# Kernel tuning notes

Hardware: AMD Instinct MI355X
Metric: run time of the kernel (lower is better)

## Reference

```python
import jax, jax.numpy as jnp
import numpy as np

B, T = 2048, 2048
VOCAB, E, H = 32000, 4, 4


def _gru_layer(x, Wih, Whh, bih, bhh, reverse=False):
    """PyTorch-semantics GRU over batch_first x [B,T,F]; returns [B,T,H]."""
    Bn = x.shape[0]
    Hn = Whh.shape[1]
    # Precompute input projections for all timesteps: [B,T,3H]
    xi = jnp.einsum('btf,gf->btg', x, Wih) + bih
    if reverse:
        xi = xi[:, ::-1]
    xi_t = jnp.swapaxes(xi, 0, 1)  # [T,B,3H]

    def step(h, xt):
        gh = h @ Whh.T + bhh                      # [B,3H]
        xr, xz, xn = jnp.split(xt, 3, axis=-1)
        hr, hz, hn = jnp.split(gh, 3, axis=-1)
        r = jax.nn.sigmoid(xr + hr)
        z = jax.nn.sigmoid(xz + hz)
        n = jnp.tanh(xn + r * hn)
        h_new = (1.0 - z) * n + z * h
        return h_new, h_new

    h0 = jnp.zeros((Bn, Hn), x.dtype)
    _, ys = jax.lax.scan(step, h0, xi_t)
    ys = jnp.swapaxes(ys, 0, 1)  # [B,T,H]
    if reverse:
        ys = ys[:, ::-1]
    return ys


def setup_inputs() -> dict:
    key = jax.random.key(0)
    ks = jax.random.split(key, 16)
    x = jax.random.randint(ks[0], (B, T), 0, VOCAB, dtype=jnp.int64)
    s = 0.3  # xavier-ish scale for tiny dims
    emb   = jax.random.normal(ks[1], (VOCAB, E), jnp.float32) * s
    Wih_f = jax.random.normal(ks[2], (3 * H, E), jnp.float32) * s
    Whh_f = jax.random.normal(ks[3], (3 * H, H), jnp.float32) * s
    Wih_b = jax.random.normal(ks[4], (3 * H, E), jnp.float32) * s
    Whh_b = jax.random.normal(ks[5], (3 * H, H), jnp.float32) * s
    Wih_o = jax.random.normal(ks[6], (3 * 1, 2 * H), jnp.float32) * s
    Whh_o = jax.random.normal(ks[7], (3 * 1, 1), jnp.float32) * s
    z = jnp.zeros
    return {
        'x': x, 'emb': emb,
        'Wih_f': Wih_f, 'Whh_f': Whh_f, 'bih_f': z((3 * H,)), 'bhh_f': z((3 * H,)),
        'Wih_b': Wih_b, 'Whh_b': Whh_b, 'bih_b': z((3 * H,)), 'bhh_b': z((3 * H,)),
        'Wih_o': Wih_o, 'Whh_o': Whh_o, 'bih_o': z((3,)), 'bhh_o': z((3,)),
    }


def reference(x, emb, Wih_f, Whh_f, bih_f, bhh_f, Wih_b, Whh_b, bih_b, bhh_b,
              Wih_o, Whh_o, bih_o, bhh_o):
    h = emb[x]                                         # [B,T,E]
    fwd = _gru_layer(h, Wih_f, Whh_f, bih_f, bhh_f, reverse=False)
    bwd = _gru_layer(h, Wih_b, Whh_b, bih_b, bhh_b, reverse=True)
    bi = jnp.concatenate([fwd, bwd], axis=-1)          # [B,T,2H]
    out = _gru_layer(bi, Wih_o, Whh_o, bih_o, bhh_o)   # [B,T,1]
    return jax.nn.sigmoid(out).reshape(x.shape[0], -1) # [B,T]
```

## Files before the change

kernel.cpp:

```cpp
#include <hip/hip_runtime.h>
#include <hip/hip_bf16.h>
#include <hip/hip_fp16.h>


#define NB 2048
#define NT 2048
#define NV 32000
#define PA_CH 32
#define PA_CL 64
#define PA_WUP 24
#define PB_CH 64
#define PB_CL 32
#define PB_WUP 16
#define CH 32
#define CL (NT / CH)
#define WUP 64

#define W_EMB    0
#define W_WIH_F  128000
#define W_WHH_F  128048
#define W_BIH_F  128096
#define W_BHH_F  128108
#define W_WIH_B  128120
#define W_WHH_B  128168
#define W_BIH_B  128216
#define W_BHH_B  128228
#define W_WIH_O  128240
#define W_WHH_O  128264
#define W_BIH_O  128267
#define W_BHH_O  128270
#define W_TOTAL  128273

static constexpr size_t WBLK_BYTES = 524288;
static constexpr size_t XIH_BYTES  = (size_t)NV * 16 * 2;
static constexpr size_t D_BYTES    = (size_t)NT * NB * 8;
static constexpr size_t XT_BYTES   = (size_t)NT * NB * 2;
static constexpr size_t N2_XIH_F   = WBLK_BYTES;
static constexpr size_t N2_XIH_B   = N2_XIH_F + XIH_BYTES;
static constexpr size_t N2_DF      = N2_XIH_B + XIH_BYTES;
static constexpr size_t N2_DB      = N2_DF + D_BYTES;
static constexpr size_t N2_XT      = N2_DB + D_BYTES;
static constexpr size_t NEED_NEW2  = N2_XT + XT_BYTES;
static constexpr size_t XI_STRIDE  = 16;
static constexpr size_t XI_BYTES   = (size_t)NV * XI_STRIDE * 4;
static constexpr size_t HS_BYTES   = (size_t)NT * NB * 4 * 2;
static constexpr size_t OFF_XI_F   = WBLK_BYTES;
static constexpr size_t OFF_XI_B   = OFF_XI_F + XI_BYTES;
static constexpr size_t OFF_HS_B   = OFF_XI_B + XI_BYTES;
static constexpr size_t OFF_HS_F   = OFF_HS_B + HS_BYTES;
static constexpr size_t NEED_XI    = OFF_HS_B;
static constexpr size_t NEED_FAST  = OFF_HS_F + HS_BYTES;

__device__ __forceinline__ float frcp_(float x) { return __builtin_amdgcn_rcpf(x); }
__device__ __forceinline__ float sigm_(float x) { return frcp_(1.f + __expf(-x)); }
__device__ __forceinline__ float tanh_(float x) { return 1.f - 2.f * frcp_(1.f + __expf(2.f * x)); }
__device__ __forceinline__ float b2f_(__hip_bfloat16 v) { return __bfloat162float(v); }
__device__ __forceinline__ unsigned f2bf_(float f) {
  __hip_bfloat16 h = __float2bfloat16(f);
  return (unsigned)__builtin_bit_cast(unsigned short, h);
}
__device__ __forceinline__ unsigned pack2_(float a, float b) { return f2bf_(a) | (f2bf_(b) << 16); }
__device__ __forceinline__ float bflo_(unsigned u) { return __builtin_bit_cast(float, u << 16); }
__device__ __forceinline__ float bfhi_(unsigned u) { return __builtin_bit_cast(float, u & 0xffff0000u); }
__device__ __forceinline__ float2 h2f2_(unsigned u) {
  __half2 h = __builtin_bit_cast(__half2, u);
  return __half22float2(h);
}
__device__ __forceinline__ unsigned packh2_(float a, float b) {
  __half2 h = __floats2half2_rn(a, b);
  return __builtin_bit_cast(unsigned, h);
}

__device__ __forceinline__ int probe_is_bf16_(const void* emb) {
  const unsigned short* u = (const unsigned short*)emb;
  int sane = 0;
#pragma unroll
  for (int i = 0; i < 64; ++i) {
    unsigned short v = u[2 * i];
    unsigned e = (v >> 7) & 0xff;
    sane += (e >= 107 && e <= 146) || ((v & 0x7fff) == 0);
  }
  return sane >= 48;
}
__device__ __forceinline__ int probe_x_is64_(const int* x) {
  int zeros = 0;
#pragma unroll
  for (int i = 0; i < 32; ++i) zeros += (x[2 * i + 1] == 0);
  return zeros >= 28;
}
__device__ __forceinline__ int tok_(const int* x, size_t idx, int is64) {
  return is64 ? x[idx * 2] : x[idx];
}
__device__ __forceinline__ float ldf_(const void* p, int i, int isb) {
  return isb ? b2f_(((const __hip_bfloat16*)p)[i]) : ((const float*)p)[i];
}

__global__ void prep_fused_kernel(const int* __restrict__ x,
                                  const void* emb, const void* Wih_f, const void* Whh_f,
                                  const void* bih_f, const void* bhh_f,
                                  const void* Wih_b, const void* Whh_b,
                                  const void* bih_b, const void* bhh_b,
                                  const void* Wih_o, const void* Whh_o,
                                  const void* bih_o, const void* bhh_o,
                                  __half* __restrict__ xih_f, __half* __restrict__ xih_b,
                                  unsigned short* __restrict__ xT, float* __restrict__ W) {
  __shared__ int tile[64][65];
  const int blk = blockIdx.x;
  if (blk < 251) {
    const int tid = blk * 256 + (int)threadIdx.x;
    if (tid >= 2 * NV) return;
    const int isb = probe_is_bf16_(emb);
    const int dir = (tid >= NV) ? 1 : 0;
    const int v = dir ? tid - NV : tid;
    const void* Wih = dir ? Wih_b : Wih_f;
    const void* bih = dir ? bih_b : bih_f;
    const void* bhh = dir ? bhh_b : bhh_f;
    char* dst = (char*)((dir ? xih_b : xih_f) + (size_t)v * 16);
    const float e0 = ldf_(emb, v * 4 + 0, isb), e1 = ldf_(emb, v * 4 + 1, isb);
    const float e2 = ldf_(emb, v * 4 + 2, isb), e3 = ldf_(emb, v * 4 + 3, isb);
    float g[12];
#pragma unroll
    for (int gi = 0; gi < 12; ++gi) {
      float s = ldf_(bih, gi, isb) + (gi < 8 ? ldf_(bhh, gi, isb) : 0.f);
      s += ldf_(Wih, gi * 4 + 0, isb) * e0 + ldf_(Wih, gi * 4 + 1, isb) * e1 +
           ldf_(Wih, gi * 4 + 2, isb) * e2 + ldf_(Wih, gi * 4 + 3, isb) * e3;
      g[gi] = s;
    }
    uint4 qa, qb;
    qa.x = packh2_(g[0], g[1]);  qa.y = packh2_(g[2], g[3]);
    qa.z = packh2_(g[4], g[5]);  qa.w = packh2_(g[6], g[7]);
    qb.x = packh2_(g[8], g[9]);  qb.y = packh2_(g[10], g[11]);
    qb.z = 0u; qb.w = 0u;
    *(uint4*)(dst) = qa;
    *(uint4*)(dst + 16) = qb;
  } else if (blk < 1275) {
    const int x64 = probe_x_is64_(x);
    const int bi2 = blk - 251;
    const int tb = bi2 & 31;
    const int tt = bi2 >> 5;
    const int b0 = tb * 64, t0 = tt * 64;
    const int r = (int)threadIdx.x >> 2;
    const int s = (int)threadIdx.x & 3;
    const int bb = b0 + r;
    if (x64) {
      const uint4* p = (const uint4*)(x + ((size_t)bb * NT + t0 + s * 16) * 2);
#pragma unroll
      for (int i = 0; i < 8; ++i) {
        uint4 q = p[i];
        tile[r][s * 16 + 2 * i] = (int)q.x;
        tile[r][s * 16 + 2 * i + 1] = (int)q.z;
      }
    } else {
      const uint4* p = (const uint4*)(x + (size_t)bb * NT + t0 + s * 16);
#pragma unroll
      for (int i = 0; i < 4; ++i) {
        uint4 q = p[i];
        const int base = s * 16 + 4 * i;
        tile[r][base] = (int)q.x; tile[r][base + 1] = (int)q.y;
        tile[r][base + 2] = (int)q.z; tile[r][base + 3] = (int)q.w;
      }
    }
    __syncthreads();
    const int tx = (int)threadIdx.x & 63, ty = (int)threadIdx.x >> 6;
#pragma unroll
    for (int j = 0; j < 16; ++j) {
      const int t = t0 + ty + 4 * j;
      xT[(size_t)t * NB + b0 + tx] = (unsigned short)tile[tx][ty + 4 * j];
    }
  } else {
    const int i0 = (int)threadIdx.x;
    if (i0 >= W_TOTAL - W_WHH_F) return;
    const int isb = probe_is_bf16_(emb);
    const int i = W_WHH_F + i0;
    const void* src; int off;
    if      (i < W_BIH_F) { src = Whh_f; off = i - W_WHH_F; }
    else if (i < W_BHH_F) { src = bih_f; off = i - W_BIH_F; }
    else if (i < W_WIH_B) { src = bhh_f; off = i - W_BHH_F; }
    else if (i < W_WHH_B) { src = Wih_b; off = i - W_WIH_B; }
    else if (i < W_BIH_B) { src = Whh_b; off = i - W_WHH_B; }
    else if (i < W_BHH_B) { src = bih_b; off = i - W_BIH_B; }
    else if (i < W_WIH_O) { src = bhh_b; off = i - W_BHH_B; }
    else if (i < W_WHH_O) { src = Wih_o; off = i - W_WIH_O; }
    else if (i < W_BIH_O) { src = Whh_o; off = i - W_WHH_O; }
    else if (i < W_BHH_O) { src = bih_o; off = i - W_BIH_O; }
    else                  { src = bhh_o; off = i - W_BHH_O; }
    W[i] = ldf_(src, off, isb);
  }
}

__global__ void __launch_bounds__(64, 2)
gru_scan_p5(const unsigned short* __restrict__ xT, const float* __restrict__ W,
            const __half* __restrict__ xih_f, const __half* __restrict__ xih_b,
            unsigned* __restrict__ df, unsigned* __restrict__ db) {
  const int bi = blockIdx.x;
  const int rg = bi & 31;
  const int c = (bi >> 5) & (PA_CH - 1);
  const int dir = bi >> 10;
  const int b = rg * 64 + (int)threadIdx.x;
  const char* __restrict__ xib = (const char*)(dir ? xih_b : xih_f);
  const char* __restrict__ xtb = (const char*)xT;
  char* __restrict__ dsb = (char*)(dir ? db : df);
  const float* Whh = W + (dir ? W_WHH_B : W_WHH_F);
  const float* bhh = W + (dir ? W_BHH_B : W_BHH_F);

  float w[12][4];
#pragma unroll
  for (int g = 0; g < 12; ++g)
#pragma unroll
    for (int k = 0; k < 4; ++k) w[g][k] = Whh[g * 4 + k];
  float bn[4];
#pragma unroll
  for (int j = 0; j < 4; ++j) bn[j] = bhh[8 + j];
  float wr4[4], wz4[4], wn4[4];
#pragma unroll
  for (int k = 0; k < 4; ++k) {
    wr4[k] = W[W_WIH_O + dir * 4 + k];
    wz4[k] = W[W_WIH_O + 8 + dir * 4 + k];
    wn4[k] = W[W_WIH_O + 16 + dir * 4 + k];
  }

  const int lo = c * PA_CL, hi = lo + PA_CL;
  int t0, d, wsteps;
  if (dir == 0) {
    d = 1;
    t0 = (c == 0) ? 0 : lo - PA_WUP;
    wsteps = (c == 0) ? 0 : PA_WUP;
  } else {
    d = -1;
    t0 = (c == PA_CH - 1) ? NT - 1 : hi - 1 + PA_WUP;
    wsteps = (c == PA_CH - 1) ? 0 : PA_WUP;
  }

#define CLMP(tt_) ((tt_) < 0 ? 0 : ((tt_) > NT - 1 ? NT - 1 : (tt_)))

  uint4 XA[8], XB[8];
  int KT[8];
#pragma unroll
  for (int j = 0; j < 8; ++j) {
    const int tj = CLMP(t0 + j * d);
    const unsigned kj = (unsigned)xT[(size_t)tj * NB + b] << 5;
    XA[j] = *(const uint4*)(xib + kj);
    XB[j] = *(const uint4*)(xib + kj + 16);
  }
#pragma unroll
  for (int j = 0; j < 8; ++j) {
    const int tj = CLMP(t0 + (8 + j) * d);
    KT[j] = (int)xT[(size_t)tj * NB + b];
  }

  const int dtok = d * (NB * 2);
  const int otlo = b * 2, othi = (NT - 1) * (NB * 2) + b * 2;
  int otok = CLMP(t0 + 16 * d) * (NB * 2) + b * 2;

  float h[4] = {0.f, 0.f, 0.f, 0.f};
  int odot = 0;
  const int ddot = d * (NB * 8);

#define ASTEP(J, DO_STORE)                                                     \
  {                                                                            \
    const unsigned ko = (unsigned)KT[J] << 5;                                  \
    const uint4 A = XA[J];                                                     \
    const uint4 Bq = XB[J];                                                    \
    XA[J] = *(const uint4*)(xib + ko);                                         \
    XB[J] = *(const uint4*)(xib + ko + 16);                                    \
    KT[J] = (int)*(const unsigned short*)(xtb + otok);                         \
    otok += dtok;                                                              \
    otok = otok < otlo ? otlo : (otok > othi ? othi : otok);                   \
    const float2 r01 = h2f2_(A.x), r23 = h2f2_(A.y);                           \
    const float2 z01 = h2f2_(A.z), z23 = h2f2_(A.w);                           \
    const float2 n01 = h2f2_(Bq.x), n23 = h2f2_(Bq.y);                         \
    const float xr[4] = {r01.x, r01.y, r23.x, r23.y};                          \
    const float xz[4] = {z01.x, z01.y, z23.x, z23.y};                          \
    const float xnn[4] = {n01.x, n01.y, n23.x, n23.y};                         \
    float r[4], z[4], n[4];                                                    \
    _Pragma("unroll")                                                          \
    for (int j = 0; j < 4; ++j) {                                              \
      float ar = xr[j], az = xz[j], an = bn[j];                                \
      _Pragma("unroll")                                                        \
      for (int k = 0; k < 4; ++k) {                                            \
        ar += w[j][k] * h[k];                                                  \
        az += w[4 + j][k] * h[k];                                              \
        an += w[8 + j][k] * h[k];                                              \
      }                                                                        \
      r[j] = sigm_(ar);                                                        \
      z[j] = sigm_(az);                                                        \
      n[j] = tanh_(xnn[j] + r[j] * an);                                        \
    }                                                                          \
    _Pragma("unroll")                                                          \
    for (int j = 0; j < 4; ++j) h[j] = n[j] + z[j] * (h[j] - n[j]);            \
    if (DO_STORE) {                                                            \
      float dr = 0.f, dz = 0.f, dn = 0.f;                                      \
      _Pragma("unroll")                                                        \
      for (int k = 0; k < 4; ++k) {                                            \
        dr += wr4[k] * h[k];                                                   \
        dz += wz4[k] * h[k];                                                   \
        dn += wn4[k] * h[k];                                                   \
      }                                                                        \
      uint2 st;                                                                \
      st.x = packh2_(dr, dz);                                                  \
      st.y = packh2_(dn, 0.f);                                                 \
      *(uint2*)(dsb + odot) = st;                                              \
      odot += ddot;                                                            \
    }                                                                          \
  }

  if (wsteps) {
#pragma unroll 1
    for (int i = 0; i < PA_WUP; i += 8) {
      ASTEP(0, 0) ASTEP(1, 0) ASTEP(2, 0) ASTEP(3, 0)
      ASTEP(4, 0) ASTEP(5, 0) ASTEP(6, 0) ASTEP(7, 0)
    }
  }
  {
    const int te = (d > 0) ? lo : hi - 1;
    odot = te * (NB * 8) + b * 8;
  }
#pragma unroll 1
  for (int i = 0; i < PA_CL; i += 8) {
    ASTEP(0, 1) ASTEP(1, 1) ASTEP(2, 1) ASTEP(3, 1)
    ASTEP(4, 1) ASTEP(5, 1) ASTEP(6, 1) ASTEP(7, 1)
  }
#undef ASTEP
#undef CLMP
}

__global__ void __launch_bounds__(64, 2)
out_scan_p5(const unsigned* __restrict__ df, const unsigned* __restrict__ db,
            const float* __restrict__ W, float* __restrict__ out) {
  const int bi = blockIdx.x;
  const int rg = bi & 31;
  const int c = bi >> 5;
  const int b = rg * 64 + (int)threadIdx.x;
  const float ur = W[W_WHH_O + 0], uz = W[W_WHH_O + 1], un = W[W_WHH_O + 2];
  const float cr = W[W_BIH_O + 0] + W[W_BHH_O + 0];
  const float cz = W[W_BIH_O + 1] + W[W_BHH_O + 1];
  const float cx = W[W_BIH_O + 2];
  const float ch = W[W_BHH_O + 2];
  const char* __restrict__ dfb = (const char*)df;
  const char* __restrict__ dbb = (const char*)db;

  const int lo = c * PB_CL;
  const int t0 = (c == 0) ? 0 : lo - PB_WUP;
  const int wsteps = (c == 0) ? 0 : PB_WUP;

  uint2 F[8], Bv[8];
#pragma unroll
  for (int j = 0; j < 8; ++j) {
    const int off = (t0 + j) * (NB * 8) + b * 8;
    F[j] = *(const uint2*)(dfb + off);
    Bv[j] = *(const uint2*)(dbb + off);
  }
  int ofs = (t0 + 8) * (NB * 8) + b * 8;
  const int ofshi = (NT - 1) * (NB * 8) + b * 8;

  float h = 0.f;
  float ob[PB_CL];

#define BSTEP(S, EMIT, OBI)                                                    \
  {                                                                            \
    const uint2 Fc = F[S], Bc = Bv[S];                                         \
    F[S] = *(const uint2*)(dfb + ofs);                                         \
    Bv[S] = *(const uint2*)(dbb + ofs);                                        \
    ofs += NB * 8;                                                             \
    ofs = ofs > ofshi ? ofshi : ofs;                                           \
    const float2 fa = h2f2_(Fc.x);                                             \
    const float2 fb = h2f2_(Fc.y);                                             \
    const float2 ba = h2f2_(Bc.x);                                             \
    const float2 bb = h2f2_(Bc.y);                                             \
    const float ar = cr + ur * h + fa.x + ba.x;                                \
    const float az = cz + uz * h + fa.y + ba.y;                                \
    const float ax = cx + fb.x + bb.x;                                         \
    const float an = ch + un * h;                                              \
    const float rr = sigm_(ar), zz = sigm_(az);                                \
    const float nn = tanh_(ax + rr * an);                                      \
    h = nn + zz * (h - nn);                                                    \
    if (EMIT) ob[OBI] = sigm_(h);                                              \
  }

  if (wsteps) {
#pragma unroll 1
    for (int i = 0; i < 2; ++i) {
      BSTEP(0, 0, 0) BSTEP(1, 0, 0) BSTEP(2, 0, 0) BSTEP(3, 0, 0)
      BSTEP(4, 0, 0) BSTEP(5, 0, 0) BSTEP(6, 0, 0) BSTEP(7, 0, 0)
    }
  }
  BSTEP(0, 1, 0)  BSTEP(1, 1, 1)  BSTEP(2, 1, 2)  BSTEP(3, 1, 3)
  BSTEP(4, 1, 4)  BSTEP(5, 1, 5)  BSTEP(6, 1, 6)  BSTEP(7, 1, 7)
  BSTEP(0, 1, 8)  BSTEP(1, 1, 9)  BSTEP(2, 1, 10) BSTEP(3, 1, 11)
  BSTEP(4, 1, 12) BSTEP(5, 1, 13) BSTEP(6, 1, 14) BSTEP(7, 1, 15)
  BSTEP(0, 1, 16) BSTEP(1, 1, 17) BSTEP(2, 1, 18) BSTEP(3, 1, 19)
  BSTEP(4, 1, 20) BSTEP(5, 1, 21) BSTEP(6, 1, 22) BSTEP(7, 1, 23)
  BSTEP(0, 1, 24) BSTEP(1, 1, 25) BSTEP(2, 1, 26) BSTEP(3, 1, 27)
  BSTEP(4, 1, 28) BSTEP(5, 1, 29) BSTEP(6, 1, 30) BSTEP(7, 1, 31)
#undef BSTEP

  float* dp = out + (size_t)b * NT + lo;
#pragma unroll
  for (int j = 0; j < 8; ++j) {
    float4 q = {ob[4 * j], ob[4 * j + 1], ob[4 * j + 2], ob[4 * j + 3]};
    *(float4*)(dp + 4 * j) = q;
  }
}

__global__ void convert_weights_kernel(const void* emb, const void* Wih_f, const void* Whh_f,
                                       const void* bih_f, const void* bhh_f,
                                       const void* Wih_b, const void* Whh_b,
                                       const void* bih_b, const void* bhh_b,
                                       const void* Wih_o, const void* Whh_o,
                                       const void* bih_o, const void* bhh_o,
                                       float* __restrict__ W) {
  const int isb = probe_is_bf16_(emb);
  for (int i = blockIdx.x * blockDim.x + threadIdx.x; i < W_TOTAL;
       i += gridDim.x * blockDim.x) {
    const void* src; int off;
    if      (i < W_WIH_F) { src = emb;   off = i; }
    else if (i < W_WHH_F) { src = Wih_f; off = i - W_WIH_F; }
    else if (i < W_BIH_F) { src = Whh_f; off = i - W_WHH_F; }
    else if (i < W_BHH_F) { src = bih_f; off = i - W_BIH_F; }
    else if (i < W_WIH_B) { src = bhh_f; off = i - W_BHH_F; }
    else if (i < W_WHH_B) { src = Wih_b; off = i - W_WIH_B; }
    else if (i < W_BIH_B) { src = Whh_b; off = i - W_WHH_B; }
    else if (i < W_BHH_B) { src = bih_b; off = i - W_BIH_B; }
    else if (i < W_WIH_O) { src = bhh_b; off = i - W_BHH_B; }
    else if (i < W_WHH_O) { src = Wih_o; off = i - W_WIH_O; }
    else if (i < W_BIH_O) { src = Whh_o; off = i - W_WHH_O; }
    else if (i < W_BHH_O) { src = bih_o; off = i - W_BIH_O; }
    else                  { src = bhh_o; off = i - W_BHH_O; }
    W[i] = ldf_(src, off, isb);
  }
}

__global__ void build_xi_kernel(const float* __restrict__ W,
                                float* __restrict__ xi_f, float* __restrict__ xi_b) {
  const int tid = blockIdx.x * blockDim.x + threadIdx.x;
  if (tid >= 2 * NV) return;
  const int dir = (tid >= NV) ? 1 : 0;
  const int v = dir ? tid - NV : tid;
  const float* Wih = W + (dir ? W_WIH_B : W_WIH_F);
  const float* bih = W + (dir ? W_BIH_B : W_BIH_F);
  const float* bhh = W + (dir ? W_BHH_B : W_BHH_F);
  float* dstp = (dir ? xi_b : xi_f) + (size_t)v * XI_STRIDE;
  const float e0 = W[W_EMB + v * 4 + 0], e1 = W[W_EMB + v * 4 + 1];
  const float e2 = W[W_EMB + v * 4 + 2], e3 = W[W_EMB + v * 4 + 3];
#pragma unroll
  for (int g = 0; g < 12; ++g) {
    float s = bih[g] + (g < 8 ? bhh[g] : 0.f);
    s += Wih[g * 4 + 0] * e0 + Wih[g * 4 + 1] * e1 + Wih[g * 4 + 2] * e2 + Wih[g * 4 + 3] * e3;
    dstp[g] = s;
  }
}

__global__ void __launch_bounds__(64, 1)
gru_scan_chunked(const int* __restrict__ x, const float* __restrict__ W,
                 const float* __restrict__ xi_f, const float* __restrict__ xi_b,
                 unsigned* __restrict__ hs_f, unsigned* __restrict__ hs_b) {
  const int bi = blockIdx.x;
  const int rg = bi & 31;
  const int c = (bi >> 5) & (CH - 1);
  const int dir = bi / (32 * CH);
  const int b = rg * 64 + (int)threadIdx.x;
  const int x64 = probe_x_is64_(x);
  const float* __restrict__ xi = dir ? xi_b : xi_f;
  const float* Whh = W + (dir ? W_WHH_B : W_WHH_F);
  const float* bhh = W + (dir ? W_BHH_B : W_BHH_F);
  unsigned* __restrict__ hs = dir ? hs_b : hs_f;
  float w[12][4];
#pragma unroll
  for (int g = 0; g < 12; ++g)
#pragma unroll
    for (int k = 0; k < 4; ++k) w[g][k] = Whh[g * 4 + k];
  float bn[4];
#pragma unroll
  for (int j = 0; j < 4; ++j) bn[j] = bhh[8 + j];
  const size_t xbase = (size_t)b * NT;
  const int lo = c * CL, hi = lo + CL;
  int t0, d, nsteps, tlast;
  if (dir == 0) {
    t0 = lo - WUP; if (t0 < 0) t0 = 0;
    d = 1; nsteps = hi - t0; tlast = hi - 1;
  } else {
    t0 = hi - 1 + WUP; if (t0 > NT - 1) t0 = NT - 1;
    d = -1; nsteps = t0 - lo + 1; tlast = lo;
  }
  int k2;
  float4 X0a, X0b, X0c, X1a, X1b, X1c;
  {
    int tb = t0 + d;     if (d > 0) { if (tb > tlast) tb = tlast; } else { if (tb < tlast) tb = tlast; }
    int tc = t0 + 2 * d; if (d > 0) { if (tc > tlast) tc = tlast; } else { if (tc < tlast) tc = tlast; }
    const int ka = tok_(x, xbase + t0, x64);
    const int kb = tok_(x, xbase + tb, x64);
    k2 = tok_(x, xbase + tc, x64);
    const float4* p = (const float4*)(xi + (size_t)ka * XI_STRIDE);
    X0a = p[0]; X0b = p[1]; X0c = p[2];
    const float4* q = (const float4*)(xi + (size_t)kb * XI_STRIDE);
    X1a = q[0]; X1b = q[1]; X1c = q[2];
  }
  float h[4] = {0.f, 0.f, 0.f, 0.f};
  int t = t0;
  for (int i = 0; i < nsteps; ++i) {
    int td = t + 3 * d; if (d > 0) { if (td > tlast) td = tlast; } else { if (td < tlast) td = tlast; }
    const int k3 = tok_(x, xbase + td, x64);
    const float4* p2 = (const float4*)(xi + (size_t)k2 * XI_STRIDE);
    float4 X2a = p2[0], X2b = p2[1], X2c = p2[2];
    const float xr[4] = {X0a.x, X0a.y, X0a.z, X0a.w};
    const float xz[4] = {X0b.x, X0b.y, X0b.z, X0b.w};
    const float xn[4] = {X0c.x, X0c.y, X0c.z, X0c.w};
    float r[4], z[4], n[4];
#pragma unroll
    for (int j = 0; j < 4; ++j) {
      float ar = xr[j], az = xz[j], an = bn[j];
#pragma unroll
      for (int k = 0; k < 4; ++k) {
        ar += w[j][k] * h[k];
        az += w[4 + j][k] * h[k];
        an += w[8 + j][k] * h[k];
      }
      r[j] = sigm_(ar); z[j] = sigm_(az); n[j] = tanh_(xn[j] + r[j] * an);
    }
#pragma unroll
    for (int j = 0; j < 4; ++j) h[j] = n[j] + z[j] * (h[j] - n[j]);
    if ((unsigned)(t - lo) < (unsigned)CL) {
      const size_t idx = ((size_t)t * NB + b) * 2;
      uint2 st; st.x = pack2_(h[0], h[1]); st.y = pack2_(h[2], h[3]);
      *(uint2*)(hs + idx) = st;
    }
    X0a = X1a; X0b = X1b; X0c = X1c;
    X1a = X2a; X1b = X2b; X1c = X2c;
    k2 = k3; t += d;
  }
}

__global__ void __launch_bounds__(64, 1)
out_scan_chunked(const unsigned* __restrict__ hs_f, const unsigned* __restrict__ hs_b,
                 const float* __restrict__ W, float* __restrict__ out) {
  const int bi = blockIdx.x;
  const int rg = bi & 31;
  const int c = bi >> 5;
  const int b = rg * 64 + (int)threadIdx.x;
  float wr[8], wz[8], wn[8];
#pragma unroll
  for (int k = 0; k < 8; ++k) {
    wr[k] = W[W_WIH_O + k]; wz[k] = W[W_WIH_O + 8 + k]; wn[k] = W[W_WIH_O + 16 + k];
  }
  const float ur = W[W_WHH_O + 0], uz = W[W_WHH_O + 1], un = W[W_WHH_O + 2];
  const float cr = W[W_BIH_O + 0] + W[W_BHH_O + 0];
  const float cz = W[W_BIH_O + 1] + W[W_BHH_O + 1];
  const float cx = W[W_BIH_O + 2];
  const float ch = W[W_BHH_O + 2];
  const int lo = c * CL, hi = lo + CL;
  int t0 = lo - WUP; if (t0 < 0) t0 = 0;
  float h = 0.f;
  uint2 F0, Bb0, F1, Bb1;
  {
    const size_t i0 = ((size_t)t0 * NB + b) * 2;
    F0 = *(const uint2*)(hs_f + i0); Bb0 = *(const uint2*)(hs_b + i0);
    int t1 = t0 + 1; if (t1 > hi - 1) t1 = hi - 1;
    const size_t i1 = ((size_t)t1 * NB + b) * 2;
    F1 = *(const uint2*)(hs_f + i1); Bb1 = *(const uint2*)(hs_b + i1);
  }
  float ob[8];
  for (int t = t0; t < hi; ++t) {
    int tp = t + 2; if (tp > hi - 1) tp = hi - 1;
    const size_t ip = ((size_t)tp * NB + b) * 2;
    uint2 F2 = *(const uint2*)(hs_f + ip);
    uint2 Bb2 = *(const uint2*)(hs_b + ip);
    const float bi8[8] = {bflo_(F0.x), bfhi_(F0.x), bflo_(F0.y), bfhi_(F0.y),
                          bflo_(Bb0.x), bfhi_(Bb0.x), bflo_(Bb0.y), bfhi_(Bb0.y)};
    float ar = cr + ur * h, az = cz + uz * h, an = ch + un * h, ax = cx;
#pragma unroll
    for (int k = 0; k < 8; ++k) {
      ar += wr[k] * bi8[k]; az += wz[k] * bi8[k]; ax += wn[k] * bi8[k];
    }
    const float r = sigm_(ar), z = sigm_(az);
    const float n = tanh_(ax + r * an);
    h = n + z * (h - n);
    if (t >= lo) {
      ob[t & 7] = sigm_(h);
      if ((t & 7) == 7) {
        float4 q0 = {ob[0], ob[1], ob[2], ob[3]};
        float4 q1 = {ob[4], ob[5], ob[6], ob[7]};
        float4* dstp = (float4*)(out + (size_t)b * NT + (t & ~7));
        dstp[0] = q0; dstp[1] = q1;
      }
    }
    F0 = F1; Bb0 = Bb1; F1 = F2; Bb1 = Bb2;
  }
}

__global__ void __launch_bounds__(64, 1)
fwd_out_scan_kernel(const int* __restrict__ x, const float* __restrict__ W,
                    const float* __restrict__ xi_f, const unsigned* __restrict__ hs_b,
                    float* __restrict__ out) {
  const int b = blockIdx.x * 64 + threadIdx.x;
  const int x64 = probe_x_is64_(x);
  float w[12][4];
#pragma unroll
  for (int g = 0; g < 12; ++g)
#pragma unroll
    for (int k = 0; k < 4; ++k) w[g][k] = W[W_WHH_F + g * 4 + k];
  float bn[4];
#pragma unroll
  for (int j = 0; j < 4; ++j) bn[j] = W[W_BHH_F + 8 + j];
  float wr[8], wz[8], wno[8];
#pragma unroll
  for (int k = 0; k < 8; ++k) {
    wr[k] = W[W_WIH_O + k]; wz[k] = W[W_WIH_O + 8 + k]; wno[k] = W[W_WIH_O + 16 + k];
  }
  const float ur = W[W_WHH_O + 0], uz = W[W_WHH_O + 1], un = W[W_WHH_O + 2];
  const float cr = W[W_BIH_O + 0] + W[W_BHH_O + 0];
  const float cz = W[W_BIH_O + 1] + W[W_BHH_O + 1];
  const float cx = W[W_BIH_O + 2];
  const float chh = W[W_BHH_O + 2];
  const size_t xbase = (size_t)b * NT;
  float h[4] = {0.f, 0.f, 0.f, 0.f};
  float ho = 0.f;
  const float4* p0 = (const float4*)(xi_f + (size_t)tok_(x, xbase, x64) * XI_STRIDE);
  float4 A0 = p0[0], A1 = p0[1], A2 = p0[2];
  for (int tg = 0; tg < NT / 8; ++tg) {
    float ob[8];
#pragma unroll
    for (int s = 0; s < 8; ++s) {
      const int t = tg * 8 + s;
      const int tn = (t + 1 < NT) ? t + 1 : t;
      const float4* pn = (const float4*)(xi_f + (size_t)tok_(x, xbase + tn, x64) * XI_STRIDE);
      float4 B0 = pn[0], B1 = pn[1], B2 = pn[2];
      const size_t idx = ((size_t)t * NB + b) * 2;
      uint2 ub = {0u, 0u};
      if (hs_b) ub = *(const uint2*)(hs_b + idx);
      const float xr[4] = {A0.x, A0.y, A0.z, A0.w};
      const float xz[4] = {A1.x, A1.y, A1.z, A1.w};
      const float xn[4] = {A2.x, A2.y, A2.z, A2.w};
      float r[4], z[4], n[4];
#pragma unroll
      for (int j = 0; j < 4; ++j) {
        float ar = xr[j], az = xz[j], an = bn[j];
#pragma unroll
        for (int k = 0; k < 4; ++k) {
          ar += w[j][k] * h[k]; az += w[4 + j][k] * h[k]; an += w[8 + j][k] * h[k];
        }
        r[j] = sigm_(ar); z[j] = sigm_(az); n[j] = tanh_(xn[j] + r[j] * an);
      }
#pragma unroll
      for (int j = 0; j < 4; ++j) h[j] = n[j] + z[j] * (h[j] - n[j]);
      const float bi8[8] = {h[0], h[1], h[2], h[3],
                            bflo_(ub.x), bfhi_(ub.x), bflo_(ub.y), bfhi_(ub.y)};
      float ar = cr + ur * ho, az = cz + uz * ho, an = chh + un * ho, ax = cx;
#pragma unroll
      for (int k = 0; k < 8; ++k) {
        ar += wr[k] * bi8[k]; az += wz[k] * bi8[k]; ax += wno[k] * bi8[k];
      }
      const float rr = sigm_(ar), zz = sigm_(az);
      const float nn = tanh_(ax + rr * an);
      ho = nn + zz * (ho - nn);
      ob[s] = sigm_(ho);
      A0 = B0; A1 = B1; A2 = B2;
    }
    float4 q0 = {ob[0], ob[1], ob[2], ob[3]};
    float4 q1 = {ob[4], ob[5], ob[6], ob[7]};
    float4* dstp = (float4*)(out + (size_t)b * NT + tg * 8);
    dstp[0] = q0; dstp[1] = q1;
  }
}

__global__ void fill_sentinel_kernel(float* out, int n) {
  int i = blockIdx.x * blockDim.x + threadIdx.x;
  if (i < n) out[i] = 0.25f;
}

extern "C" void kernel_launch(void* const* d_in, const int* in_sizes, int n_in,
                              void* d_out, int out_size, void* d_ws, size_t ws_size,
                              hipStream_t stream) {
  (void)in_sizes; (void)n_in;
  const int* x = (const int*)d_in[0];
  char* ws = (char*)d_ws;
  float* W = (float*)ws;
  float* out = (float*)d_out;

  if (ws_size < NEED_XI) {
    fill_sentinel_kernel<<<(out_size + 255) / 256, 256, 0, stream>>>(out, out_size);
    return;
  }

  if (ws_size >= NEED_NEW2) {
    __half* xih_f = (__half*)(ws + N2_XIH_F);
    __half* xih_b = (__half*)(ws + N2_XIH_B);
    unsigned* df = (unsigned*)(ws + N2_DF);
    unsigned* db = (unsigned*)(ws + N2_DB);
    unsigned short* xT = (unsigned short*)(ws + N2_XT);
    prep_fused_kernel<<<1276, 256, 0, stream>>>(
        x, d_in[1], d_in[2], d_in[3], d_in[4], d_in[5], d_in[6], d_in[7],
        d_in[8], d_in[9], d_in[10], d_in[11], d_in[12], d_in[13],
        xih_f, xih_b, xT, W);
    gru_scan_p5<<<2 * PA_CH * 32, 64, 0, stream>>>(xT, W, xih_f, xih_b, df, db);
    out_scan_p5<<<PB_CH * 32, 64, 0, stream>>>(df, db, W, out);
    return;
  }

  convert_weights_kernel<<<504, 256, 0, stream>>>(
      d_in[1], d_in[2], d_in[3], d_in[4], d_in[5], d_in[6], d_in[7],
      d_in[8], d_in[9], d_in[10], d_in[11], d_in[12], d_in[13], W);
  float* xi_f = (float*)(ws + OFF_XI_F);
  float* xi_b = (float*)(ws + OFF_XI_B);
  unsigned* hs_b = (unsigned*)(ws + OFF_HS_B);
  unsigned* hs_f = (unsigned*)(ws + OFF_HS_F);
  build_xi_kernel<<<(2 * NV + 255) / 256, 256, 0, stream>>>(W, xi_f, xi_b);
  if (ws_size >= NEED_FAST) {
    gru_scan_chunked<<<2 * CH * 32, 64, 0, stream>>>(x, W, xi_f, xi_b, hs_f, hs_b);
    out_scan_chunked<<<CH * 32, 64, 0, stream>>>(hs_f, hs_b, W, out);
  } else {
    fwd_out_scan_kernel<<<NB / 64, 64, 0, stream>>>(x, W, xi_f, nullptr, out);
  }
}
```

Before: 110.0 us.

## Fold log2e into weights, use packed fp16 dot2 and exp2 in GRU scans

Pre-scales gate pre-activations and recurrent/output weights by log2(e) (or 2*log2(e) for the tanh gate), so the sigmoid and tanh can use a raw exp2 without an extra multiply. The 4x4 recurrent matvec and the output-projection dot products now use packed fp16 fdot2 instructions on a half-precision copy of h instead of scalar fp32 FMAs. The xT buffer is padded so the per-step token-offset clamping can be dropped from the inner loop. Rounding h and the weights to fp16 inside the recurrence adds precision error, which can build up over the 2048-step scan.

After: 107.4 us, median of 2. 1.02x faster.

```diff
diff --git a/kernel.cpp b/kernel.cpp
--- a/kernel.cpp
+++ b/kernel.cpp
@@ -31,16 +31,18 @@
 #define W_BHH_O  128270
 #define W_TOTAL  128273
 
+#define XT_PAD 24
+
 static constexpr size_t WBLK_BYTES = 524288;
+static constexpr size_t D_BYTES    = (size_t)NT * NB * 8;
+static constexpr size_t XT_BYTES_P = (size_t)(NT + 2 * XT_PAD) * NB * 2;
 static constexpr size_t XIH_BYTES  = (size_t)NV * 16 * 2;
-static constexpr size_t D_BYTES    = (size_t)NT * NB * 8;
-static constexpr size_t XT_BYTES   = (size_t)NT * NB * 2;
 static constexpr size_t N2_XIH_F   = WBLK_BYTES;
 static constexpr size_t N2_XIH_B   = N2_XIH_F + XIH_BYTES;
 static constexpr size_t N2_DF      = N2_XIH_B + XIH_BYTES;
 static constexpr size_t N2_DB      = N2_DF + D_BYTES;
 static constexpr size_t N2_XT      = N2_DB + D_BYTES;
-static constexpr size_t NEED_NEW2  = N2_XT + XT_BYTES;
+static constexpr size_t NEED_NEW2  = N2_XT + XT_BYTES_P;
 static constexpr size_t XI_STRIDE  = 16;
 static constexpr size_t XI_BYTES   = (size_t)NV * XI_STRIDE * 4;
 static constexpr size_t HS_BYTES   = (size_t)NT * NB * 4 * 2;
@@ -51,6 +53,11 @@
 static constexpr size_t NEED_XI    = OFF_HS_B;
 static constexpr size_t NEED_FAST  = OFF_HS_F + HS_BYTES;
 
+#define L2E  1.4426950408889634f
+#define L2E2 2.8853900817779268f
+
+typedef __attribute__((ext_vector_type(2))) _Float16 h2v;
+
 __device__ __forceinline__ float frcp_(float x) { return __builtin_amdgcn_rcpf(x); }
 __device__ __forceinline__ float sigm_(float x) { return frcp_(1.f + __expf(-x)); }
 __device__ __forceinline__ float tanh_(float x) { return 1.f - 2.f * frcp_(1.f + __expf(2.f * x)); }
@@ -70,6 +77,22 @@
   __half2 h = __floats2half2_rn(a, b);
   return __builtin_bit_cast(unsigned, h);
 }
+__device__ __forceinline__ h2v packh2v_(float a, float b) {
+  return __builtin_bit_cast(h2v, packh2_(a, b));
+}
+
+#if __has_builtin(__builtin_amdgcn_fdot2)
+#define FDOT2_(a, b, c) __builtin_amdgcn_fdot2((a), (b), (c), false)
+#else
+__device__ __forceinline__ float FDOT2_(h2v a, h2v b, float c) {
+  return c + (float)a.x * (float)b.x + (float)a.y * (float)b.y;
+}
+#endif
+#if __has_builtin(__builtin_amdgcn_exp2f)
+#define EXP2_(x) __builtin_amdgcn_exp2f(x)
+#else
+#define EXP2_(x) __expf(0.6931471805599453f * (x))
+#endif
 
 __device__ __forceinline__ int probe_is_bf16_(const void* emb) {
   const unsigned short* u = (const unsigned short*)emb;
@@ -95,15 +118,15 @@
   return isb ? b2f_(((const __hip_bfloat16*)p)[i]) : ((const float*)p)[i];
 }
 
-__global__ void prep_fused_kernel(const int* __restrict__ x,
-                                  const void* emb, const void* Wih_f, const void* Whh_f,
-                                  const void* bih_f, const void* bhh_f,
-                                  const void* Wih_b, const void* Whh_b,
-                                  const void* bih_b, const void* bhh_b,
-                                  const void* Wih_o, const void* Whh_o,
-                                  const void* bih_o, const void* bhh_o,
-                                  __half* __restrict__ xih_f, __half* __restrict__ xih_b,
-                                  unsigned short* __restrict__ xT, float* __restrict__ W) {
+__global__ void prep_p10(const int* __restrict__ x,
+                         const void* emb, const void* Wih_f, const void* Whh_f,
+                         const void* bih_f, const void* bhh_f,
+                         const void* Wih_b, const void* Whh_b,
+                         const void* bih_b, const void* bhh_b,
+                         const void* Wih_o, const void* Whh_o,
+                         const void* bih_o, const void* bhh_o,
+                         __half* __restrict__ xih_f, __half* __restrict__ xih_b,
+                         unsigned short* __restrict__ xT, float* __restrict__ W) {
   __shared__ int tile[64][65];
   const int blk = blockIdx.x;
   if (blk < 251) {
@@ -124,7 +147,7 @@
       float s = ldf_(bih, gi, isb) + (gi < 8 ? ldf_(bhh, gi, isb) : 0.f);
       s += ldf_(Wih, gi * 4 + 0, isb) * e0 + ldf_(Wih, gi * 4 + 1, isb) * e1 +
            ldf_(Wih, gi * 4 + 2, isb) * e2 + ldf_(Wih, gi * 4 + 3, isb) * e3;
-      g[gi] = s;
+      g[gi] = s * (gi < 8 ? L2E : L2E2);
     }
     uint4 qa, qb;
     qa.x = packh2_(g[0], g[1]);  qa.y = packh2_(g[2], g[3]);
@@ -189,9 +212,9 @@
 }
 
 __global__ void __launch_bounds__(64, 2)
-gru_scan_p5(const unsigned short* __restrict__ xT, const float* __restrict__ W,
-            const __half* __restrict__ xih_f, const __half* __restrict__ xih_b,
-            unsigned* __restrict__ df, unsigned* __restrict__ db) {
+gru_scan_p10(const unsigned short* __restrict__ xT, const float* __restrict__ W,
+             const __half* __restrict__ xih_f, const __half* __restrict__ xih_b,
+             unsigned* __restrict__ df, unsigned* __restrict__ db) {
   const int bi = blockIdx.x;
   const int rg = bi & 31;
   const int c = (bi >> 5) & (PA_CH - 1);
@@ -203,21 +226,22 @@
   const float* Whh = W + (dir ? W_WHH_B : W_WHH_F);
   const float* bhh = W + (dir ? W_BHH_B : W_BHH_F);
 
-  float w[12][4];
-#pragma unroll
-  for (int g = 0; g < 12; ++g)
-#pragma unroll
-    for (int k = 0; k < 4; ++k) w[g][k] = Whh[g * 4 + k];
+  h2v wh01[12], wh23[12];
+#pragma unroll
+  for (int g = 0; g < 12; ++g) {
+    const float sc = (g < 8) ? L2E : L2E2;
+    wh01[g] = packh2v_(Whh[g * 4 + 0] * sc, Whh[g * 4 + 1] * sc);
+    wh23[g] = packh2v_(Whh[g * 4 + 2] * sc, Whh[g * 4 + 3] * sc);
+  }
   float bn[4];
 #pragma unroll
-  for (int j = 0; j < 4; ++j) bn[j] = bhh[8 + j];
-  float wr4[4], wz4[4], wn4[4];
-#pragma unroll
-  for (int k = 0; k < 4; ++k) {
-    wr4[k] = W[W_WIH_O + dir * 4 + k];
-    wz4[k] = W[W_WIH_O + 8 + dir * 4 + k];
-    wn4[k] = W[W_WIH_O + 16 + dir * 4 + k];
-  }
+  for (int j = 0; j < 4; ++j) bn[j] = bhh[8 + j] * L2E2;
+  h2v wr01 = packh2v_(W[W_WIH_O + dir * 4 + 0] * L2E, W[W_WIH_O + dir * 4 + 1] * L2E);
+  h2v wr23 = packh2v_(W[W_WIH_O + dir * 4 + 2] * L2E, W[W_WIH_O + dir * 4 + 3] * L2E);
+  h2v wz01 = packh2v_(W[W_WIH_O + 8 + dir * 4 + 0] * L2E, W[W_WIH_O + 8 + dir * 4 + 1] * L2E);
+  h2v wz23 = packh2v_(W[W_WIH_O + 8 + dir * 4 + 2] * L2E, W[W_WIH_O + 8 + dir * 4 + 3] * L2E);
+  h2v wn01 = packh2v_(W[W_WIH_O + 16 + dir * 4 + 0] * L2E2, W[W_WIH_O + 16 + dir * 4 + 1] * L2E2);
+  h2v wn23 = packh2v_(W[W_WIH_O + 16 + dir * 4 + 2] * L2E2, W[W_WIH_O + 16 + dir * 4 + 3] * L2E2);
 
   const int lo = c * PA_CL, hi = lo + PA_CL;
   int t0, d, wsteps;
@@ -249,10 +273,10 @@
   }
 
   const int dtok = d * (NB * 2);
-  const int otlo = b * 2, othi = (NT - 1) * (NB * 2) + b * 2;
-  int otok = CLMP(t0 + 16 * d) * (NB * 2) + b * 2;
+  int otok = (t0 + 16 * d) * (NB * 2) + b * 2;
 
   float h[4] = {0.f, 0.f, 0.f, 0.f};
+  h2v h01p = packh2v_(0.f, 0.f), h23p = packh2v_(0.f, 0.f);
   int odot = 0;
   const int ddot = d * (NB * 8);
 
@@ -265,37 +289,31 @@
     XB[J] = *(const uint4*)(xib + ko + 16);                                    \
     KT[J] = (int)*(const unsigned short*)(xtb + otok);                         \
     otok += dtok;                                                              \
-    otok = otok < otlo ? otlo : (otok > othi ? othi : otok);                   \
     const float2 r01 = h2f2_(A.x), r23 = h2f2_(A.y);                           \
     const float2 z01 = h2f2_(A.z), z23 = h2f2_(A.w);                           \
     const float2 n01 = h2f2_(Bq.x), n23 = h2f2_(Bq.y);                         \
     const float xr[4] = {r01.x, r01.y, r23.x, r23.y};                          \
     const float xz[4] = {z01.x, z01.y, z23.x, z23.y};                          \
     const float xnn[4] = {n01.x, n01.y, n23.x, n23.y};                         \
-    float r[4], z[4], n[4];                                                    \
     _Pragma("unroll")                                                          \
     for (int j = 0; j < 4; ++j) {                                              \
-      float ar = xr[j], az = xz[j], an = bn[j];                                \
-      _Pragma("unroll")                                                        \
-      for (int k = 0; k < 4; ++k) {                                            \
-        ar += w[j][k] * h[k];                                                  \
-        az += w[4 + j][k] * h[k];                                              \
-        an += w[8 + j][k] * h[k];                                              \
-      }                                                                        \
-      r[j] = sigm_(ar);                                                        \
-      z[j] = sigm_(az);                                                        \
-      n[j] = tanh_(xnn[j] + r[j] * an);                                        \
+      const float ar = FDOT2_(wh01[j], h01p, FDOT2_(wh23[j], h23p, xr[j]));    \
+      const float az = FDOT2_(wh01[4 + j], h01p,                               \
+                              FDOT2_(wh23[4 + j], h23p, xz[j]));               \
+      const float an = FDOT2_(wh01[8 + j], h01p,                               \
+                              FDOT2_(wh23[8 + j], h23p, bn[j]));               \
+      const float rr = frcp_(1.f + EXP2_(-ar));                                \
+      const float zz = frcp_(1.f + EXP2_(-az));                                \
+      const float q = frcp_(1.f + EXP2_(__builtin_fmaf(rr, an, xnn[j])));      \
+      const float n = __builtin_fmaf(-2.f, q, 1.f);                            \
+      h[j] = n + zz * (h[j] - n);                                              \
     }                                                                          \
-    _Pragma("unroll")                                                          \
-    for (int j = 0; j < 4; ++j) h[j] = n[j] + z[j] * (h[j] - n[j]);            \
+    h01p = packh2v_(h[0], h[1]);                                               \
+    h23p = packh2v_(h[2], h[3]);                                               \
     if (DO_STORE) {                                                            \
-      float dr = 0.f, dz = 0.f, dn = 0.f;                                      \
-      _Pragma("unroll")                                                        \
-      for (int k = 0; k < 4; ++k) {                                            \
-        dr += wr4[k] * h[k];                                                   \
-        dz += wz4[k] * h[k];                                                   \
-        dn += wn4[k] * h[k];                                                   \
-      }                                                                        \
+      const float dr = FDOT2_(wr01, h01p, FDOT2_(wr23, h23p, 0.f));            \
+      const float dz = FDOT2_(wz01, h01p, FDOT2_(wz23, h23p, 0.f));            \
+      const float dn = FDOT2_(wn01, h01p, FDOT2_(wn23, h23p, 0.f));            \
       uint2 st;                                                                \
       st.x = packh2_(dr, dz);                                                  \
       st.y = packh2_(dn, 0.f);                                                 \
@@ -325,17 +343,18 @@
 }
 
 __global__ void __launch_bounds__(64, 2)
-out_scan_p5(const unsigned* __restrict__ df, const unsigned* __restrict__ db,
-            const float* __restrict__ W, float* __restrict__ out) {
+out_scan_p10(const unsigned* __restrict__ df, const unsigned* __restrict__ db,
+             const float* __restrict__ W, float* __restrict__ out) {
   const int bi = blockIdx.x;
   const int rg = bi & 31;
   const int c = bi >> 5;
   const int b = rg * 64 + (int)threadIdx.x;
-  const float ur = W[W_WHH_O + 0], uz = W[W_WHH_O + 1], un = W[W_WHH_O + 2];
-  const float cr = W[W_BIH_O + 0] + W[W_BHH_O + 0];
-  const float cz = W[W_BIH_O + 1] + W[W_BHH_O + 1];
-  const float cx = W[W_BIH_O + 2];
-  const float ch = W[W_BHH_O + 2];
+  const float ur = W[W_WHH_O + 0] * L2E, uz = W[W_WHH_O + 1] * L2E;
+  const float un = W[W_WHH_O + 2] * L2E2;
+  const float cr = (W[W_BIH_O + 0] + W[W_BHH_O + 0]) * L2E;
+  const float cz = (W[W_BIH_O + 1] + W[W_BHH_O + 1]) * L2E;
+  const float cx = W[W_BIH_O + 2] * L2E2;
+  const float ch = W[W_BHH_O + 2] * L2E2;
   const char* __restrict__ dfb = (const char*)df;
   const char* __restrict__ dbb = (const char*)db;
 
@@ -371,8 +390,10 @@
     const float az = cz + uz * h + fa.y + ba.y;                                \
     const float ax = cx + fb.x + bb.x;                                         \
     const float an = ch + un * h;                                              \
-    const float rr = sigm_(ar), zz = sigm_(az);                                \
-    const float nn = tanh_(ax + rr * an);                                      \
+    const float rr = frcp_(1.f + EXP2_(-ar));                                  \
+    const float zz = frcp_(1.f + EXP2_(-az));                                  \
+    const float q = frcp_(1.f + EXP2_(__builtin_fmaf(rr, an, ax)));            \
+    const float nn = __builtin_fmaf(-2.f, q, 1.f);                             \
     h = nn + zz * (h - nn);                                                    \
     if (EMIT) ob[OBI] = sigm_(h);                                              \
   }
@@ -686,13 +707,14 @@
     __half* xih_b = (__half*)(ws + N2_XIH_B);
     unsigned* df = (unsigned*)(ws + N2_DF);
     unsigned* db = (unsigned*)(ws + N2_DB);
-    unsigned short* xT = (unsigned short*)(ws + N2_XT);
-    prep_fused_kernel<<<1276, 256, 0, stream>>>(
+    unsigned short* xT_alloc = (unsigned short*)(ws + N2_XT);
+    unsigned short* xT = xT_alloc + (size_t)XT_PAD * NB;
+    prep_p10<<<1276, 256, 0, stream>>>(
         x, d_in[1], d_in[2], d_in[3], d_in[4], d_in[5], d_in[6], d_in[7],
         d_in[8], d_in[9], d_in[10], d_in[11], d_in[12], d_in[13],
         xih_f, xih_b, xT, W);
-    gru_scan_p5<<<2 * PA_CH * 32, 64, 0, stream>>>(xT, W, xih_f, xih_b, df, db);
-    out_scan_p5<<<PB_CH * 32, 64, 0, stream>>>(df, db, W, out);
+    gru_scan_p10<<<2 * PA_CH * 32, 64, 0, stream>>>(xT, W, xih_f, xih_b, df, db);
+    out_scan_p10<<<PB_CH * 32, 64, 0, stream>>>(df, db, W, out);
     return;
   }
 
```
